# Performance work log

Hardware: AMD Instinct MI355X
Metric: run time of the kernel (lower is better)

The kernel has to match this reference:

```python
import jax, jax.numpy as jnp
import numpy as np

N = 20000      # nodes
E = 320000     # edges (avg degree 16)
IN = 64        # input feature dim
EMB = 128      # emb_dim / c_dim
OUT = 10       # num classes
L = 5          # num_layers
RATIO = 0.25
TEMP = 1.0
NOISE = 1.0
MAX_ITER = 30
EPS = 1e-20


def setup_inputs() -> dict:
    key = jax.random.key(0)
    ks = jax.random.split(key, 12)
    def w(k, shape, fan):
        return jax.random.normal(k, shape, jnp.float32) / np.float32(np.sqrt(fan))
    x = jax.random.normal(ks[0], (N, IN), jnp.float32)
    edge_index = jax.random.randint(ks[1], (2, E), 0, N, jnp.int32)
    u = jax.random.uniform(ks[2], (E, 1), jnp.float32)
    return {
        "x": x,
        "edge_index": edge_index,
        "u": u,
        "enc_W0": w(ks[3], (IN, EMB), IN), "enc_b0": jnp.zeros((EMB,), jnp.float32),
        "enc_W": w(ks[4], (L - 1, EMB, EMB), EMB), "enc_b": jnp.zeros((L - 1, EMB), jnp.float32),
        "ea_W1": w(ks[5], (2 * EMB, 4 * EMB), 2 * EMB), "ea_b1": jnp.zeros((4 * EMB,), jnp.float32),
        "ea_W2": w(ks[6], (4 * EMB, 1), 4 * EMB), "ea_b2": jnp.zeros((1,), jnp.float32),
        "cls_W0": w(ks[7], (IN, EMB), IN), "cls_b0": jnp.zeros((EMB,), jnp.float32),
        "cls_W": w(ks[8], (L - 1, EMB, EMB), EMB), "cls_b": jnp.zeros((L - 1, EMB), jnp.float32),
        "head_W": w(ks[9], (EMB, OUT), EMB), "head_b": jnp.zeros((OUT,), jnp.float32),
    }


def _gin_stack(x, W0, b0, Ws, bs, src, dst, att):
    """GIN-style stack: aggregate att-weighted neighbor messages, then linear+ReLU."""
    agg = jax.ops.segment_sum(x[src] * att, dst, num_segments=N)
    h = jax.nn.relu((x + agg) @ W0 + b0)
    def layer(h, wb):
        W, b = wb
        agg = jax.ops.segment_sum(h[src] * att, dst, num_segments=N)
        return jax.nn.relu((h + agg) @ W + b), None
    h, _ = jax.lax.scan(layer, h, (Ws, bs))
    return h


def reference(x, edge_index, u, enc_W0, enc_b0, enc_W, enc_b,
              ea_W1, ea_b1, ea_W2, ea_b2,
              cls_W0, cls_b0, cls_W, cls_b, head_W, head_b):
    src, dst = edge_index[0], edge_index[1]
    ones = jnp.ones((E, 1), jnp.float32)

    # GNN encoder
    h = _gin_stack(x, enc_W0, enc_b0, enc_W, enc_b, src, dst, ones)

    # edge attention MLP on [h_src, h_dst]
    edge_rep = jnp.concatenate([h[src], h[dst]], axis=-1)            # [E, 2*EMB]
    pe = jax.nn.relu(edge_rep @ ea_W1 + ea_b1) @ ea_W2 + ea_b2       # [E, 1]
    atts = (pe - pe.mean()) / jnp.std(pe, ddof=1)

    # Gumbel noise from uniform u (training path)
    g = -jnp.log(-jnp.log(u + EPS) + EPS)
    d = atts + g * NOISE

    s_min, s_max = atts.min(), atts.max()
    D = jnp.concatenate([d - s_min, s_max - d], axis=-1)             # [E, 2]
    logT = -D / TEMP
    log_rs = jnp.log(jnp.array([[E * (1.0 - RATIO), E * RATIO]], jnp.float32) + EPS)

    # 30-step Sinkhorn normalization in log space
    def body(i, lt):
        lt = lt - jax.scipy.special.logsumexp(lt, axis=-1, keepdims=True)
        lt = lt - jax.scipy.special.logsumexp(lt, axis=-2, keepdims=True)
        return lt + log_rs
    logT = jax.lax.fori_loop(0, MAX_ITER, body, logT)
    T = jnp.exp(logT)[:, 1:2]                                        # [E, 1]

    # classifier GNN on raw features with Sinkhorn edge attention
    hc = _gin_stack(x, cls_W0, cls_b0, cls_W, cls_b, src, dst, T)
    rep = hc.mean(axis=0)                                            # mean graph pooling
    return rep @ head_W + head_b                                     # [OUT]
```

## Files before the change

### kernel.cpp

```cpp
#include <hip/hip_runtime.h>
#include <math.h>

#define NN 20000
#define EE 320000
#define NBINS 2048
#define HRANGE 64.0f
#define EPSF 1e-20f

typedef __attribute__((ext_vector_type(8))) short bf16x8;
typedef __attribute__((ext_vector_type(4))) float f32x4;

constexpr size_t OFF_DEG  = 0;
constexpr size_t OFF_RS   = 20000;
constexpr size_t OFF_CUR  = 40008;
constexpr size_t OFF_EIX  = 60008;
constexpr size_t OFF_GSRC = 380008;
constexpr size_t OFF_B0   = 700008;
constexpr size_t OFF_B1   = 1980008;
constexpr size_t OFF_PA   = 3260008;
constexpr size_t OFF_PB   = 8380008;
constexpr size_t OFF_PE   = 13500008;
constexpr size_t OFF_DL   = 13820008;
constexpr size_t OFF_TT   = 14140008;
constexpr size_t OFF_HIST = 14460008;
constexpr size_t OFF_SCAL = 14464104;
constexpr size_t OFF_REP  = 14464136;
constexpr size_t OFF_WT   = 14464264;
constexpr size_t WT_ENC0 = 0;
constexpr size_t WT_ENC  = 8192;
constexpr size_t WT_CLS0 = 73728;
constexpr size_t WT_CLS  = 81920;
constexpr size_t WT_EA1  = 147456;

__device__ __forceinline__ unsigned ordf(float f) {
  unsigned b = __float_as_uint(f);
  return (b >> 31) ? ~b : (b | 0x80000000u);
}
__device__ __forceinline__ float unordf(unsigned u) {
  unsigned b = (u >> 31) ? (u ^ 0x80000000u) : ~u;
  return __uint_as_float(b);
}
__device__ __forceinline__ ushort f2bf(float f) {
  unsigned u = __float_as_uint(f);
  u += 0x7FFFu + ((u >> 16) & 1u);
  return (ushort)(u >> 16);
}
__device__ __forceinline__ unsigned pack2(float x, float y) {
  return (unsigned)f2bf(x) | ((unsigned)f2bf(y) << 16);
}
__device__ __forceinline__ float bf2f(ushort h) {
  return __uint_as_float(((unsigned)h) << 16);
}
__device__ __forceinline__ float bflo(unsigned v) { return __uint_as_float(v << 16); }
__device__ __forceinline__ float bfhi(unsigned v) { return __uint_as_float(v & 0xFFFF0000u); }

__global__ void init_ws(int* deg, int* cur, float* hist, float* scal, float* rep) {
  int i = blockIdx.x * blockDim.x + threadIdx.x;
  if (i < NN) { deg[i] = 0; cur[i] = 0; }
  if (i < 2 * NBINS) hist[i] = 0.f;
  if (i < 128) rep[i] = 0.f;
  if (i < 32) {
    if (i == 2)      ((unsigned*)scal)[2] = 0xFFFFFFFFu;
    else if (i == 3) ((unsigned*)scal)[3] = 0u;
    else scal[i] = 0.f;
  }
}

__global__ void count_deg(const int* __restrict__ dst, int* __restrict__ deg) {
  int e = blockIdx.x * 256 + threadIdx.x;
  if (e < EE) atomicAdd(&deg[dst[e]], 1);
}

__global__ __launch_bounds__(1024) void scan_deg(const int* __restrict__ deg,
                                                 int* __restrict__ rs) {
  __shared__ int ps[1024];
  const int t = threadIdx.x;
  const int base = t * 20;
  int loc[20];
  int s = 0;
#pragma unroll
  for (int j = 0; j < 20; ++j) {
    int idx = base + j;
    int v = (idx < NN) ? deg[idx] : 0;
    loc[j] = s;
    s += v;
  }
  ps[t] = s;
  __syncthreads();
  for (int off = 1; off < 1024; off <<= 1) {
    int x = (t >= off) ? ps[t - off] : 0;
    __syncthreads();
    ps[t] += x;
    __syncthreads();
  }
  const int excl = ps[t] - s;
#pragma unroll
  for (int j = 0; j < 20; ++j) {
    int idx = base + j;
    if (idx < NN) rs[idx] = excl + loc[j];
  }
  if (t == 1023) rs[NN] = ps[1023];
}

__global__ void fill_csr(const int* __restrict__ src, const int* __restrict__ dst,
                         const int* __restrict__ rs, int* __restrict__ cur,
                         int* __restrict__ eidx, int* __restrict__ gsrc) {
  int e = blockIdx.x * 256 + threadIdx.x;
  if (e < EE) {
    int d = dst[e];
    int p = atomicAdd(&cur[d], 1);
    int o = rs[d] + p;
    eidx[o] = e;
    gsrc[o] = src[e];
  }
}

__global__ void transpose_all(const float* __restrict__ encW0, const float* __restrict__ encW,
                              const float* __restrict__ clsW0, const float* __restrict__ clsW,
                              const float* __restrict__ eaW1, ushort* __restrict__ Wt) {
  int i = blockIdx.x * 256 + threadIdx.x;
  if (i < 8192) {
    int k = i >> 7, n = i & 127;
    Wt[WT_ENC0 + n * 64 + k] = f2bf(encW0[i]);
  } else if (i < 73728) {
    int j = i - 8192;
    int l = j >> 14, r = j & 16383, k = r >> 7, n = r & 127;
    Wt[WT_ENC + l * 16384 + n * 128 + k] = f2bf(encW[j]);
  } else if (i < 81920) {
    int j = i - 73728;
    int k = j >> 7, n = j & 127;
    Wt[WT_CLS0 + n * 64 + k] = f2bf(clsW0[j]);
  } else if (i < 147456) {
    int j = i - 81920;
    int l = j >> 14, r = j & 16383, k = r >> 7, n = r & 127;
    Wt[WT_CLS + l * 16384 + n * 128 + k] = f2bf(clsW[j]);
  } else if (i < 278528) {
    int j = i - 147456;
    int k = j >> 9, n = j & 511;
    Wt[WT_EA1 + n * 256 + k] = f2bf(eaW1[j]);
  }
}

template <bool HASATT>
__global__ __launch_bounds__(256) void fused_layer64(
    const float* __restrict__ X, ushort* __restrict__ C,
    const int* __restrict__ gsrc, const int* __restrict__ rs,
    const float* __restrict__ att, const ushort* __restrict__ Bt,
    const float* __restrict__ bias) {
  __shared__ __align__(16) char smem[8448];
  ushort* Asm = (ushort*)smem;
  const int tid = threadIdx.x;
  const int g = tid >> 4, l = tid & 15;
  const int nb = blockIdx.x * 16;
  {
    const int n = nb + g;
    const int e0 = rs[n];
    const int deg = rs[n + 1] - e0;
    float4 s = ((const float4*)(X + (size_t)n * 64))[l];
    float a[4] = {s.x, s.y, s.z, s.w};
    const float4* Xr = (const float4*)X;

    int i0 = gsrc[min(e0 + 0, EE - 1)];
    int i1 = gsrc[min(e0 + 1, EE - 1)];
    int i2 = gsrc[min(e0 + 2, EE - 1)];
    int i3 = gsrc[min(e0 + 3, EE - 1)];
    float4 F0 = Xr[(size_t)i0 * 16 + l];
    float4 F1 = Xr[(size_t)i1 * 16 + l];
    float4 F2 = Xr[(size_t)i2 * 16 + l];
    float4 F3 = Xr[(size_t)i3 * 16 + l];
    int G0 = gsrc[min(e0 + 4, EE - 1)];
    int G1 = gsrc[min(e0 + 5, EE - 1)];
    int G2 = gsrc[min(e0 + 6, EE - 1)];
    int G3 = gsrc[min(e0 + 7, EE - 1)];
    float W0 = 1.f, W1 = 1.f, W2 = 1.f, W3 = 1.f;
    if (HASATT) {
      W0 = att[min(e0 + 0, EE - 1)];
      W1 = att[min(e0 + 1, EE - 1)];
      W2 = att[min(e0 + 2, EE - 1)];
      W3 = att[min(e0 + 3, EE - 1)];
    }

#define FL64_STEP(F, G, W, J)                                                 \
    {                                                                         \
      if ((J) < deg) {                                                        \
        const float cw_ = HASATT ? (W) : 1.f;                                 \
        a[0] = fmaf(cw_, F.x, a[0]); a[1] = fmaf(cw_, F.y, a[1]);             \
        a[2] = fmaf(cw_, F.z, a[2]); a[3] = fmaf(cw_, F.w, a[3]);             \
      }                                                                       \
      F = Xr[(size_t)G * 16 + l];                                             \
      G = gsrc[min(e0 + (J) + 8, EE - 1)];                                    \
      if (HASATT) W = att[min(e0 + (J) + 4, EE - 1)];                         \
    }

    for (int j = 0; j < deg; j += 4) {
      FL64_STEP(F0, G0, W0, j);
      FL64_STEP(F1, G1, W1, j + 1);
      FL64_STEP(F2, G2, W2, j + 2);
      FL64_STEP(F3, G3, W3, j + 3);
    }
#undef FL64_STEP
    ushort4 o;
    o.x = f2bf(a[0]); o.y = f2bf(a[1]); o.z = f2bf(a[2]); o.w = f2bf(a[3]);
    *(ushort4*)(Asm + g * 72 + l * 4) = o;
  }
  __syncthreads();
  const int wave = tid >> 6, lane = tid & 63, quad = lane >> 4, l15 = lane & 15;
  f32x4 acc[2] = {{0.f, 0.f, 0.f, 0.f}, {0.f, 0.f, 0.f, 0.f}};
#pragma unroll
  for (int k0 = 0; k0 < 64; k0 += 32) {
    bf16x8 af = *(const bf16x8*)(Asm + l15 * 72 + k0 + quad * 8);
#pragma unroll
    for (int t = 0; t < 2; ++t) {
      int bn = wave * 32 + t * 16 + l15;
      bf16x8 bf = *(const bf16x8*)(Bt + (size_t)bn * 64 + k0 + quad * 8);
      acc[t] = __builtin_amdgcn_mfma_f32_16x16x32_bf16(af, bf, acc[t], 0, 0, 0);
    }
  }
  __syncthreads();
  float (*Csm)[132] = (float(*)[132])smem;
#pragma unroll
  for (int t = 0; t < 2; ++t) {
    int lc = wave * 32 + t * 16 + l15;
    float bs = bias[lc];
#pragma unroll
    for (int r = 0; r < 4; ++r)
      Csm[quad * 4 + r][lc] = fmaxf(acc[t][r] + bs, 0.f);
  }
  __syncthreads();
  const int r = tid >> 4, cc = (tid & 15) * 8;
  f32x4 v0 = *(const f32x4*)&Csm[r][cc];
  f32x4 v1 = *(const f32x4*)&Csm[r][cc + 4];
  uint4 o;
  o.x = pack2(v0[0], v0[1]); o.y = pack2(v0[2], v0[3]);
  o.z = pack2(v1[0], v1[1]); o.w = pack2(v1[2], v1[3]);
  *(uint4*)(C + (size_t)(nb + r) * 128 + cc) = o;
}

template <bool HASATT>
__global__ __launch_bounds__(256) void fused_layer128(
    const ushort* __restrict__ Xb, ushort* __restrict__ C,
    const int* __restrict__ gsrc, const int* __restrict__ rs,
    const float* __restrict__ att, const ushort* __restrict__ Bt,
    const float* __restrict__ bias) {
  __shared__ __align__(16) char smem[8448];
  ushort* Asm = (ushort*)smem;
  const int tid = threadIdx.x;
  const int g = tid >> 4, l = tid & 15;
  const int nb = blockIdx.x * 16;
  {
    const int n = nb + g;
    const int e0 = rs[n];
    const int deg = rs[n + 1] - e0;
    float a[8];
    {
      uint4 s = ((const uint4*)(Xb + (size_t)n * 128))[l];
      a[0] = bflo(s.x); a[1] = bfhi(s.x); a[2] = bflo(s.y); a[3] = bfhi(s.y);
      a[4] = bflo(s.z); a[5] = bfhi(s.z); a[6] = bflo(s.w); a[7] = bfhi(s.w);
    }
    const uint4* Xr = (const uint4*)Xb;

    int i0 = gsrc[min(e0 + 0, EE - 1)];
    int i1 = gsrc[min(e0 + 1, EE - 1)];
    int i2 = gsrc[min(e0 + 2, EE - 1)];
    int i3 = gsrc[min(e0 + 3, EE - 1)];
    uint4 F0 = Xr[(size_t)i0 * 16 + l];
    uint4 F1 = Xr[(size_t)i1 * 16 + l];
    uint4 F2 = Xr[(size_t)i2 * 16 + l];
    uint4 F3 = Xr[(size_t)i3 * 16 + l];
    int G0 = gsrc[min(e0 + 4, EE - 1)];
    int G1 = gsrc[min(e0 + 5, EE - 1)];
    int G2 = gsrc[min(e0 + 6, EE - 1)];
    int G3 = gsrc[min(e0 + 7, EE - 1)];
    float W0 = 1.f, W1 = 1.f, W2 = 1.f, W3 = 1.f;
    if (HASATT) {
      W0 = att[min(e0 + 0, EE - 1)];
      W1 = att[min(e0 + 1, EE - 1)];
      W2 = att[min(e0 + 2, EE - 1)];
      W3 = att[min(e0 + 3, EE - 1)];
    }

#define FL128_STEP(F, G, W, J)                                                \
    {                                                                         \
      if ((J) < deg) {                                                        \
        const float cw_ = HASATT ? (W) : 1.f;                                 \
        a[0] = fmaf(cw_, bflo(F.x), a[0]); a[1] = fmaf(cw_, bfhi(F.x), a[1]); \
        a[2] = fmaf(cw_, bflo(F.y), a[2]); a[3] = fmaf(cw_, bfhi(F.y), a[3]); \
        a[4] = fmaf(cw_, bflo(F.z), a[4]); a[5] = fmaf(cw_, bfhi(F.z), a[5]); \
        a[6] = fmaf(cw_, bflo(F.w), a[6]); a[7] = fmaf(cw_, bfhi(F.w), a[7]); \
      }                                                                       \
      F = Xr[(size_t)G * 16 + l];                                             \
      G = gsrc[min(e0 + (J) + 8, EE - 1)];                                    \
      if (HASATT) W = att[min(e0 + (J) + 4, EE - 1)];                         \
    }

    for (int j = 0; j < deg; j += 4) {
      FL128_STEP(F0, G0, W0, j);
      FL128_STEP(F1, G1, W1, j + 1);
      FL128_STEP(F2, G2, W2, j + 2);
      FL128_STEP(F3, G3, W3, j + 3);
    }
#undef FL128_STEP
    uint4 o;
    o.x = pack2(a[0], a[1]); o.y = pack2(a[2], a[3]);
    o.z = pack2(a[4], a[5]); o.w = pack2(a[6], a[7]);
    *(uint4*)(Asm + g * 136 + l * 8) = o;
  }
  __syncthreads();
  const int wave = tid >> 6, lane = tid & 63, quad = lane >> 4, l15 = lane & 15;
  f32x4 acc[2] = {{0.f, 0.f, 0.f, 0.f}, {0.f, 0.f, 0.f, 0.f}};
#pragma unroll
  for (int k0 = 0; k0 < 128; k0 += 32) {
    bf16x8 af = *(const bf16x8*)(Asm + l15 * 136 + k0 + quad * 8);
#pragma unroll
    for (int t = 0; t < 2; ++t) {
      int bn = wave * 32 + t * 16 + l15;
      bf16x8 bf = *(const bf16x8*)(Bt + (size_t)bn * 128 + k0 + quad * 8);
      acc[t] = __builtin_amdgcn_mfma_f32_16x16x32_bf16(af, bf, acc[t], 0, 0, 0);
    }
  }
  __syncthreads();
  float (*Csm)[132] = (float(*)[132])smem;
#pragma unroll
  for (int t = 0; t < 2; ++t) {
    int lc = wave * 32 + t * 16 + l15;
    float bs = bias[lc];
#pragma unroll
    for (int r = 0; r < 4; ++r)
      Csm[quad * 4 + r][lc] = fmaxf(acc[t][r] + bs, 0.f);
  }
  __syncthreads();
  const int r = tid >> 4, cc = (tid & 15) * 8;
  f32x4 v0 = *(const f32x4*)&Csm[r][cc];
  f32x4 v1 = *(const f32x4*)&Csm[r][cc + 4];
  uint4 o;
  o.x = pack2(v0[0], v0[1]); o.y = pack2(v0[2], v0[3]);
  o.z = pack2(v1[0], v1[1]); o.w = pack2(v1[2], v1[3]);
  *(uint4*)(C + (size_t)(nb + r) * 128 + cc) = o;
}

__global__ __launch_bounds__(256) void gemm_papb(
    const ushort* __restrict__ Hb, const ushort* __restrict__ W1t,
    const float* __restrict__ b1, ushort* __restrict__ Pa, ushort* __restrict__ Pb) {
  __shared__ float lds[32][132];
  const int tid = threadIdx.x;
  const int wave = tid >> 6, lane = tid & 63, quad = lane >> 4, l15 = lane & 15;
  const int mh = wave >> 1, nh = wave & 1;
  const bool isB = blockIdx.x >= 4;
  const int col0 = (blockIdx.x & 3) * 128;
  const int row0 = blockIdx.y * 32;
  const ushort* Bt = W1t + (isB ? 128 : 0);
  ushort* C = isB ? Pb : Pa;
  f32x4 acc[4] = {{0.f, 0.f, 0.f, 0.f}, {0.f, 0.f, 0.f, 0.f},
                  {0.f, 0.f, 0.f, 0.f}, {0.f, 0.f, 0.f, 0.f}};
  const ushort* Ap = Hb + (size_t)(row0 + mh * 16 + l15) * 128 + quad * 8;
#pragma unroll
  for (int k0 = 0; k0 < 128; k0 += 32) {
    bf16x8 af = *(const bf16x8*)(Ap + k0);
#pragma unroll
    for (int t = 0; t < 4; ++t) {
      int bn = col0 + nh * 64 + t * 16 + l15;
      bf16x8 bf = *(const bf16x8*)(Bt + (size_t)bn * 256 + k0 + quad * 8);
      acc[t] = __builtin_amdgcn_mfma_f32_16x16x32_bf16(af, bf, acc[t], 0, 0, 0);
    }
  }
#pragma unroll
  for (int t = 0; t < 4; ++t) {
    int lc = nh * 64 + t * 16 + l15;
    float bs = isB ? 0.f : b1[col0 + lc];
#pragma unroll
    for (int r = 0; r < 4; ++r)
      lds[mh * 16 + quad * 4 + r][lc] = acc[t][r] + bs;
  }
  __syncthreads();
  const int r = tid >> 3, c0 = (tid & 7) * 16;
  ushort* Cp = C + (size_t)(row0 + r) * 512 + col0 + c0;
#pragma unroll
  for (int k = 0; k < 4; ++k) {
    f32x4 v = *(const f32x4*)&lds[r][c0 + k * 4];
    ushort4 o;
    o.x = f2bf(v[0]); o.y = f2bf(v[1]); o.z = f2bf(v[2]); o.w = f2bf(v[3]);
    *(ushort4*)(Cp + k * 4) = o;
  }
}

__global__ __launch_bounds__(256) void edge_pe_csr(
    const ushort* __restrict__ Pa, const ushort* __restrict__ Pb,
    const int* __restrict__ gsrc, const int* __restrict__ rs,
    const float* __restrict__ W2, const float* __restrict__ b2,
    float* __restrict__ pe) {
  const int lane = threadIdx.x & 63;
  const int n = blockIdx.x * 4 + (threadIdx.x >> 6);
  const int e0 = rs[n];
  const int deg = rs[n + 1] - e0;
  if (deg <= 0) return;
  float w[8], pb[8];
  {
    const float4* w2v = (const float4*)(W2 + lane * 8);
    float4 t0 = w2v[0], t1 = w2v[1];
    w[0] = t0.x; w[1] = t0.y; w[2] = t0.z; w[3] = t0.w;
    w[4] = t1.x; w[5] = t1.y; w[6] = t1.z; w[7] = t1.w;
    uint4 b = ((const uint4*)(Pb + (size_t)n * 512))[lane];
    pb[0] = bflo(b.x); pb[1] = bfhi(b.x); pb[2] = bflo(b.y); pb[3] = bfhi(b.y);
    pb[4] = bflo(b.z); pb[5] = bfhi(b.z); pb[6] = bflo(b.w); pb[7] = bfhi(b.w);
  }
  const float b2v = b2[0];
  const uint4* Par = (const uint4*)Pa;

  int i0 = gsrc[min(e0 + 0, EE - 1)];
  int i1 = gsrc[min(e0 + 1, EE - 1)];
  int i2 = gsrc[min(e0 + 2, EE - 1)];
  int i3 = gsrc[min(e0 + 3, EE - 1)];
  uint4 F0 = Par[(size_t)i0 * 64 + lane];
  uint4 F1 = Par[(size_t)i1 * 64 + lane];
  uint4 F2 = Par[(size_t)i2 * 64 + lane];
  uint4 F3 = Par[(size_t)i3 * 64 + lane];
  int G0 = gsrc[min(e0 + 4, EE - 1)];
  int G1 = gsrc[min(e0 + 5, EE - 1)];
  int G2 = gsrc[min(e0 + 6, EE - 1)];
  int G3 = gsrc[min(e0 + 7, EE - 1)];

#define PE_STEP(F, G, J)                                                      \
  {                                                                           \
    if ((J) < deg) {                                                          \
      float pa[8] = {bflo(F.x), bfhi(F.x), bflo(F.y), bfhi(F.y),              \
                     bflo(F.z), bfhi(F.z), bflo(F.w), bfhi(F.w)};             \
      float acc = 0.f;                                                        \
      _Pragma("unroll")                                                       \
      for (int jj = 0; jj < 8; ++jj) acc += fmaxf(pa[jj] + pb[jj], 0.f) * w[jj]; \
      _Pragma("unroll")                                                       \
      for (int off = 32; off; off >>= 1) acc += __shfl_xor(acc, off);         \
      if (lane == 0) pe[e0 + (J)] = acc + b2v;                                \
    }                                                                         \
    F = Par[(size_t)G * 64 + lane];                                           \
    G = gsrc[min(e0 + (J) + 8, EE - 1)];                                      \
  }

  for (int j = 0; j < deg; j += 4) {
    PE_STEP(F0, G0, j);
    PE_STEP(F1, G1, j + 1);
    PE_STEP(F2, G2, j + 2);
    PE_STEP(F3, G3, j + 3);
  }
#undef PE_STEP
}

__global__ __launch_bounds__(256) void pe_stats(const float* __restrict__ pe,
                                                float* __restrict__ scal) {
  __shared__ float r1[256], r2[256], r3[256], r4[256];
  int tid = threadIdx.x;
  float s = 0.f, q = 0.f, mn = 3.0e38f, mx = -3.0e38f;
  for (int i = blockIdx.x * 256 + tid; i < EE; i += gridDim.x * 256) {
    float v = pe[i];
    s += v; q = fmaf(v, v, q);
    mn = fminf(mn, v); mx = fmaxf(mx, v);
  }
  r1[tid] = s; r2[tid] = q; r3[tid] = mn; r4[tid] = mx;
  __syncthreads();
  for (int k = 128; k > 0; k >>= 1) {
    if (tid < k) {
      r1[tid] += r1[tid + k];
      r2[tid] += r2[tid + k];
      r3[tid] = fminf(r3[tid], r3[tid + k]);
      r4[tid] = fmaxf(r4[tid], r4[tid + k]);
    }
    __syncthreads();
  }
  if (tid == 0) {
    unsafeAtomicAdd(&scal[0], r1[0]);
    unsafeAtomicAdd(&scal[1], r2[0]);
    atomicMin((unsigned*)scal + 2, ordf(r3[0]));
    atomicMax((unsigned*)scal + 3, ordf(r4[0]));
  }
}

__global__ __launch_bounds__(256) void edge_delta_hist(
    const float* __restrict__ pe, const float* __restrict__ u,
    const int* __restrict__ eidx, float* __restrict__ delta,
    float* __restrict__ hist, const float* __restrict__ scal) {
  __shared__ float cnt_s[NBINS], sum_s[NBINS];
  for (int b = threadIdx.x; b < NBINS; b += 256) { cnt_s[b] = 0.f; sum_s[b] = 0.f; }
  float sum = scal[0], ssq = scal[1];
  float mn = unordf(((const unsigned*)scal)[2]);
  float mx = unordf(((const unsigned*)scal)[3]);
  float mu = sum / (float)EE;
  float var = (ssq - sum * sum / (float)EE) / (float)(EE - 1);
  float istd = rsqrtf(fmaxf(var, 1e-30f));
  float shift = (mn - mu) * istd + (mx - mu) * istd;
  __syncthreads();
  for (int i = blockIdx.x * 256 + threadIdx.x; i < EE; i += gridDim.x * 256) {
    float uu = u[eidx[i]];
    float atts = (pe[i] - mu) * istd;
    float g = -logf(-logf(uu + EPSF) + EPSF);
    float dl = 2.0f * (atts + g) - shift;
    delta[i] = dl;
    float dcl = fminf(fmaxf(dl, -HRANGE), HRANGE * 0.9999f);
    int b = (int)((dcl + HRANGE) * ((float)NBINS / (2.0f * HRANGE)));
    b = min(max(b, 0), NBINS - 1);
    atomicAdd(&cnt_s[b], 1.0f);
    atomicAdd(&sum_s[b], dcl);
  }
  __syncthreads();
  for (int b = threadIdx.x; b < NBINS; b += 256) {
    float c = cnt_s[b];
    if (c != 0.f) {
      unsafeAtomicAdd(&hist[b], c);
      unsafeAtomicAdd(&hist[NBINS + b], sum_s[b]);
    }
  }
}

__global__ __launch_bounds__(64) void sinkhorn_iter(const float* __restrict__ hist,
                                                    float* __restrict__ scal) {
  const int lane = threadIdx.x;
  float cnt[32], mean[32];
#pragma unroll
  for (int b = 0; b < 32; ++b) {
    int idx = b * 64 + lane;
    float c = hist[idx];
    cnt[b] = c;
    mean[b] = (c > 0.f) ? hist[NBINS + idx] / c : 0.f;
  }
  const float LRD = -1.0986122886681098f;
  float S = 0.f, Zfin = 0.f;
  for (int it = 0; it < 30; ++it) {
    float p = 0.f;
#pragma unroll
    for (int b = 0; b < 32; ++b)
      if (cnt[b] > 0.f) p += cnt[b] / (1.f + expf(-(mean[b] + S)));
#pragma unroll
    for (int off = 32; off; off >>= 1) p += __shfl_xor(p, off);
    if (it < 29)
      S += logf(fmaxf((float)EE - p, 1.0f)) - logf(p) + LRD;
    else
      Zfin = p;
  }
  if (lane == 0) {
    scal[8] = S;
    scal[9] = ((float)EE * 0.25f) / Zfin;
  }
}

__global__ void compute_T(const float* __restrict__ delta,
                          const float* __restrict__ scal,
                          float* __restrict__ Ta) {
  int i = blockIdx.x * 256 + threadIdx.x;
  if (i >= EE) return;
  float S = scal[8], sc = scal[9];
  Ta[i] = sc / (1.f + expf(-(delta[i] + S)));
}

__global__ __launch_bounds__(128) void col_mean(const ushort* __restrict__ Hc,
                                                float* __restrict__ rep) {
  int c = threadIdx.x;
  const int g = gridDim.x;
  float p0 = 0.f, p1 = 0.f, p2 = 0.f, p3 = 0.f;
  int n = blockIdx.x;
  for (; n + 3 * g < NN; n += 4 * g) {
    p0 += bf2f(Hc[(size_t)n * 128 + c]);
    p1 += bf2f(Hc[(size_t)(n + g) * 128 + c]);
    p2 += bf2f(Hc[(size_t)(n + 2 * g) * 128 + c]);
    p3 += bf2f(Hc[(size_t)(n + 3 * g) * 128 + c]);
  }
  for (; n < NN; n += g) p0 += bf2f(Hc[(size_t)n * 128 + c]);
  unsafeAtomicAdd(&rep[c], (p0 + p1) + (p2 + p3));
}

__global__ __launch_bounds__(128) void head_kernel(const float* __restrict__ repsum,
                                                   const float* __restrict__ hW,
                                                   const float* __restrict__ hb,
                                                   float* __restrict__ out) {
  __shared__ float rep[128];
  int tid = threadIdx.x;
  if (tid < 128) rep[tid] = repsum[tid] * (1.0f / (float)NN);
  __syncthreads();
  if (tid < 10) {
    float a = hb[tid];
#pragma unroll
    for (int c = 0; c < 128; c++) a = fmaf(rep[c], hW[c * 10 + tid], a);
    out[tid] = a;
  }
}

extern "C" void kernel_launch(void* const* d_in, const int* in_sizes, int n_in,
                              void* d_out, int out_size, void* d_ws, size_t ws_size,
                              hipStream_t stream) {
  const float* x      = (const float*)d_in[0];
  const int*   ei     = (const int*)d_in[1];
  const float* u      = (const float*)d_in[2];
  const float* enc_W0 = (const float*)d_in[3];
  const float* enc_b0 = (const float*)d_in[4];
  const float* enc_W  = (const float*)d_in[5];
  const float* enc_b  = (const float*)d_in[6];
  const float* ea_W1  = (const float*)d_in[7];
  const float* ea_b1  = (const float*)d_in[8];
  const float* ea_W2  = (const float*)d_in[9];
  const float* ea_b2  = (const float*)d_in[10];
  const float* cls_W0 = (const float*)d_in[11];
  const float* cls_b0 = (const float*)d_in[12];
  const float* cls_W  = (const float*)d_in[13];
  const float* cls_b  = (const float*)d_in[14];
  const float* head_W = (const float*)d_in[15];
  const float* head_b = (const float*)d_in[16];
  const int* src  = ei;
  const int* dstp = ei + EE;

  float* wsF = (float*)d_ws;
  int*   wsI = (int*)d_ws;
  int* deg  = wsI + OFF_DEG;
  int* rs   = wsI + OFF_RS;
  int* cur  = wsI + OFF_CUR;
  int* eix  = wsI + OFF_EIX;
  int* gsrc = wsI + OFF_GSRC;
  ushort* B0 = (ushort*)(wsF + OFF_B0);
  ushort* B1 = (ushort*)(wsF + OFF_B1);
  ushort* Pa = (ushort*)(wsF + OFF_PA);
  ushort* Pb = (ushort*)(wsF + OFF_PB);
  float* pe   = wsF + OFF_PE;
  float* dl   = wsF + OFF_DL;
  float* Ta   = wsF + OFF_TT;
  float* hist = wsF + OFF_HIST;
  float* scal = wsF + OFF_SCAL;
  float* rep  = wsF + OFF_REP;
  ushort* Wt  = (ushort*)(wsF + OFF_WT);
  float* out = (float*)d_out;

  init_ws<<<(NN + 255) / 256, 256, 0, stream>>>(deg, cur, hist, scal, rep);
  count_deg<<<(EE + 255) / 256, 256, 0, stream>>>(dstp, deg);
  scan_deg<<<1, 1024, 0, stream>>>(deg, rs);
  fill_csr<<<(EE + 255) / 256, 256, 0, stream>>>(src, dstp, rs, cur, eix, gsrc);
  transpose_all<<<1088, 256, 0, stream>>>(enc_W0, enc_W, cls_W0, cls_W, ea_W1, Wt);

  const int GB = NN / 16;

  fused_layer64<false><<<GB, 256, 0, stream>>>(x, B0, gsrc, rs, nullptr, Wt + WT_ENC0, enc_b0);
  {
    ushort* in = B0; ushort* outb = B1;
    for (int l = 0; l < 4; l++) {
      fused_layer128<false><<<GB, 256, 0, stream>>>(in, outb, gsrc, rs, nullptr,
                                                    Wt + WT_ENC + (size_t)l * 16384,
                                                    enc_b + (size_t)l * 128);
      ushort* t = in; in = outb; outb = t;
    }
  }

  gemm_papb<<<dim3(8, NN / 32), 256, 0, stream>>>(B0, Wt + WT_EA1, ea_b1, Pa, Pb);
  edge_pe_csr<<<NN / 4, 256, 0, stream>>>(Pa, Pb, gsrc, rs, ea_W2, ea_b2, pe);

  pe_stats<<<512, 256, 0, stream>>>(pe, scal);
  edge_delta_hist<<<128, 256, 0, stream>>>(pe, u, eix, dl, hist, scal);
  sinkhorn_iter<<<1, 64, 0, stream>>>(hist, scal);
  compute_T<<<(EE + 255) / 256, 256, 0, stream>>>(dl, scal, Ta);

  fused_layer64<true><<<GB, 256, 0, stream>>>(x, B0, gsrc, rs, Ta, Wt + WT_CLS0, cls_b0);
  {
    ushort* in = B0; ushort* outb = B1;
    for (int l = 0; l < 4; l++) {
      fused_layer128<true><<<GB, 256, 0, stream>>>(in, outb, gsrc, rs, Ta,
                                                   Wt + WT_CLS + (size_t)l * 16384,
                                                   cls_b + (size_t)l * 128);
      ushort* t = in; in = outb; outb = t;
    }
  }

  col_mean<<<256, 128, 0, stream>>>(B0, rep);
  head_kernel<<<1, 128, 0, stream>>>(rep, head_W, head_b, out);
}
```

Measured before the change: 535.8 us.

## Compute edge attention scores with one thread per edge instead of one wave per node

Replaces the wave-per-destination-node edge scoring kernel, which used cross-lane shuffles and per-node gathers, with a thread-per-edge kernel. Each thread walks the full 512-wide Pa and Pb rows itself and accumulates the ReLU dot product. To support this, the CSR fill now also writes a per-edge destination array, stored in the T buffer region, which is only written later. This removes the shuffle reductions and the load imbalance from uneven degrees. In exchange, each thread makes strided, uncoalesced 16-byte loads across rows and no longer reuses Pb across edges held in registers, so memory efficiency depends on cache hits.

```diff
diff --git a/kernel.cpp b/kernel.cpp
--- a/kernel.cpp
+++ b/kernel.cpp
@@ -104,7 +104,8 @@
 
 __global__ void fill_csr(const int* __restrict__ src, const int* __restrict__ dst,
                          const int* __restrict__ rs, int* __restrict__ cur,
-                         int* __restrict__ eidx, int* __restrict__ gsrc) {
+                         int* __restrict__ eidx, int* __restrict__ gsrc,
+                         int* __restrict__ gdst) {
   int e = blockIdx.x * 256 + threadIdx.x;
   if (e < EE) {
     int d = dst[e];
@@ -112,6 +113,7 @@
     int o = rs[d] + p;
     eidx[o] = e;
     gsrc[o] = src[e];
+    gdst[o] = d;
   }
 }
 
@@ -385,63 +387,31 @@
 
 __global__ __launch_bounds__(256) void edge_pe_csr(
     const ushort* __restrict__ Pa, const ushort* __restrict__ Pb,
-    const int* __restrict__ gsrc, const int* __restrict__ rs,
+    const int* __restrict__ gsrc, const int* __restrict__ gdst,
     const float* __restrict__ W2, const float* __restrict__ b2,
     float* __restrict__ pe) {
-  const int lane = threadIdx.x & 63;
-  const int n = blockIdx.x * 4 + (threadIdx.x >> 6);
-  const int e0 = rs[n];
-  const int deg = rs[n + 1] - e0;
-  if (deg <= 0) return;
-  float w[8], pb[8];
-  {
-    const float4* w2v = (const float4*)(W2 + lane * 8);
-    float4 t0 = w2v[0], t1 = w2v[1];
-    w[0] = t0.x; w[1] = t0.y; w[2] = t0.z; w[3] = t0.w;
-    w[4] = t1.x; w[5] = t1.y; w[6] = t1.z; w[7] = t1.w;
-    uint4 b = ((const uint4*)(Pb + (size_t)n * 512))[lane];
-    pb[0] = bflo(b.x); pb[1] = bfhi(b.x); pb[2] = bflo(b.y); pb[3] = bfhi(b.y);
-    pb[4] = bflo(b.z); pb[5] = bfhi(b.z); pb[6] = bflo(b.w); pb[7] = bfhi(b.w);
-  }
-  const float b2v = b2[0];
-  const uint4* Par = (const uint4*)Pa;
-
-  int i0 = gsrc[min(e0 + 0, EE - 1)];
-  int i1 = gsrc[min(e0 + 1, EE - 1)];
-  int i2 = gsrc[min(e0 + 2, EE - 1)];
-  int i3 = gsrc[min(e0 + 3, EE - 1)];
-  uint4 F0 = Par[(size_t)i0 * 64 + lane];
-  uint4 F1 = Par[(size_t)i1 * 64 + lane];
-  uint4 F2 = Par[(size_t)i2 * 64 + lane];
-  uint4 F3 = Par[(size_t)i3 * 64 + lane];
-  int G0 = gsrc[min(e0 + 4, EE - 1)];
-  int G1 = gsrc[min(e0 + 5, EE - 1)];
-  int G2 = gsrc[min(e0 + 6, EE - 1)];
-  int G3 = gsrc[min(e0 + 7, EE - 1)];
-
-#define PE_STEP(F, G, J)                                                      \
-  {                                                                           \
-    if ((J) < deg) {                                                          \
-      float pa[8] = {bflo(F.x), bfhi(F.x), bflo(F.y), bfhi(F.y),              \
-                     bflo(F.z), bfhi(F.z), bflo(F.w), bfhi(F.w)};             \
-      float acc = 0.f;                                                        \
-      _Pragma("unroll")                                                       \
-      for (int jj = 0; jj < 8; ++jj) acc += fmaxf(pa[jj] + pb[jj], 0.f) * w[jj]; \
-      _Pragma("unroll")                                                       \
-      for (int off = 32; off; off >>= 1) acc += __shfl_xor(acc, off);         \
-      if (lane == 0) pe[e0 + (J)] = acc + b2v;                                \
-    }                                                                         \
-    F = Par[(size_t)G * 64 + lane];                                           \
-    G = gsrc[min(e0 + (J) + 8, EE - 1)];                                      \
-  }
-
-  for (int j = 0; j < deg; j += 4) {
-    PE_STEP(F0, G0, j);
-    PE_STEP(F1, G1, j + 1);
-    PE_STEP(F2, G2, j + 2);
-    PE_STEP(F3, G3, j + 3);
-  }
-#undef PE_STEP
+  const int e = blockIdx.x * 256 + threadIdx.x;
+  const int s = gsrc[e], d = gdst[e];
+  const uint4* Par = (const uint4*)(Pa + (size_t)s * 512);
+  const uint4* Pbr = (const uint4*)(Pb + (size_t)d * 512);
+  const float4* Wv = (const float4*)W2;
+  float a0 = 0.f, a1 = 0.f, a2 = 0.f, a3 = 0.f;
+#pragma unroll 8
+  for (int c = 0; c < 64; ++c) {
+    uint4 pa = Par[c];
+    uint4 pb = Pbr[c];
+    float4 w0 = Wv[c * 2], w1 = Wv[c * 2 + 1];
+    float t;
+    t = fmaxf(bflo(pa.x) + bflo(pb.x), 0.f); a0 = fmaf(t, w0.x, a0);
+    t = fmaxf(bfhi(pa.x) + bfhi(pb.x), 0.f); a1 = fmaf(t, w0.y, a1);
+    t = fmaxf(bflo(pa.y) + bflo(pb.y), 0.f); a2 = fmaf(t, w0.z, a2);
+    t = fmaxf(bfhi(pa.y) + bfhi(pb.y), 0.f); a3 = fmaf(t, w0.w, a3);
+    t = fmaxf(bflo(pa.z) + bflo(pb.z), 0.f); a0 = fmaf(t, w1.x, a0);
+    t = fmaxf(bfhi(pa.z) + bfhi(pb.z), 0.f); a1 = fmaf(t, w1.y, a1);
+    t = fmaxf(bflo(pa.w) + bflo(pb.w), 0.f); a2 = fmaf(t, w1.z, a2);
+    t = fmaxf(bfhi(pa.w) + bfhi(pb.w), 0.f); a3 = fmaf(t, w1.w, a3);
+  }
+  pe[e] = ((a0 + a1) + (a2 + a3)) + b2[0];
 }
 
 __global__ __launch_bounds__(256) void pe_stats(const float* __restrict__ pe,
@@ -611,6 +581,7 @@
   int* cur  = wsI + OFF_CUR;
   int* eix  = wsI + OFF_EIX;
   int* gsrc = wsI + OFF_GSRC;
+  int* gdst = wsI + OFF_TT;
   ushort* B0 = (ushort*)(wsF + OFF_B0);
   ushort* B1 = (ushort*)(wsF + OFF_B1);
   ushort* Pa = (ushort*)(wsF + OFF_PA);
@@ -627,7 +598,7 @@
   init_ws<<<(NN + 255) / 256, 256, 0, stream>>>(deg, cur, hist, scal, rep);
   count_deg<<<(EE + 255) / 256, 256, 0, stream>>>(dstp, deg);
   scan_deg<<<1, 1024, 0, stream>>>(deg, rs);
-  fill_csr<<<(EE + 255) / 256, 256, 0, stream>>>(src, dstp, rs, cur, eix, gsrc);
+  fill_csr<<<(EE + 255) / 256, 256, 0, stream>>>(src, dstp, rs, cur, eix, gsrc, gdst);
   transpose_all<<<1088, 256, 0, stream>>>(enc_W0, enc_W, cls_W0, cls_W, ea_W1, Wt);
 
   const int GB = NN / 16;
@@ -644,7 +615,7 @@
   }
 
   gemm_papb<<<dim3(8, NN / 32), 256, 0, stream>>>(B0, Wt + WT_EA1, ea_b1, Pa, Pb);
-  edge_pe_csr<<<NN / 4, 256, 0, stream>>>(Pa, Pb, gsrc, rs, ea_W2, ea_b2, pe);
+  edge_pe_csr<<<EE / 256, 256, 0, stream>>>(Pa, Pb, gsrc, gdst, ea_W2, ea_b2, pe);
 
   pe_stats<<<512, 256, 0, stream>>>(pe, scal);
   edge_delta_hist<<<128, 256, 0, stream>>>(pe, u, eix, dl, hist, scal);
```

Result: slower. 547.3 us (+2.1%).

## Assign one wavefront per node in GIN layers with quad-split edge gathering

Applied to the files above, without the earlier changes.

The fused aggregate-plus-GEMM layer kernels now process 4 nodes per block instead of 16. Each wavefront owns one node, and its four 16-lane quads walk interleaved edge subsets, then combine their partial sums with cross-lane shuffles. This targets load imbalance from varying node degrees, which previously made whole waves wait on the slowest of four nodes. The cost is that the 16-row MFMA tile now carries only 4 useful rows, there are four times as many blocks reloading the weight tile, and each lane has less gather prefetch depth.

```diff
diff --git a/kernel.cpp b/kernel.cpp
--- a/kernel.cpp
+++ b/kernel.cpp
@@ -150,61 +150,54 @@
   __shared__ __align__(16) char smem[8448];
   ushort* Asm = (ushort*)smem;
   const int tid = threadIdx.x;
-  const int g = tid >> 4, l = tid & 15;
-  const int nb = blockIdx.x * 16;
+  const int wave = tid >> 6, lane = tid & 63;
+  const int c = lane & 15;
+  const int q = lane >> 4;
+  const int nb = blockIdx.x * 4;
   {
-    const int n = nb + g;
-    const int e0 = rs[n];
-    const int deg = rs[n + 1] - e0;
-    float4 s = ((const float4*)(X + (size_t)n * 64))[l];
-    float a[4] = {s.x, s.y, s.z, s.w};
+    const int n = nb + wave;
+    const int e0 = rs[n], e1 = rs[n + 1];
+    const int deg = e1 - e0;
     const float4* Xr = (const float4*)X;
-
-    int i0 = gsrc[min(e0 + 0, EE - 1)];
-    int i1 = gsrc[min(e0 + 1, EE - 1)];
-    int i2 = gsrc[min(e0 + 2, EE - 1)];
-    int i3 = gsrc[min(e0 + 3, EE - 1)];
-    float4 F0 = Xr[(size_t)i0 * 16 + l];
-    float4 F1 = Xr[(size_t)i1 * 16 + l];
-    float4 F2 = Xr[(size_t)i2 * 16 + l];
-    float4 F3 = Xr[(size_t)i3 * 16 + l];
-    int G0 = gsrc[min(e0 + 4, EE - 1)];
-    int G1 = gsrc[min(e0 + 5, EE - 1)];
-    int G2 = gsrc[min(e0 + 6, EE - 1)];
-    int G3 = gsrc[min(e0 + 7, EE - 1)];
-    float W0 = 1.f, W1 = 1.f, W2 = 1.f, W3 = 1.f;
+    float a[4];
+    {
+      float4 s = Xr[(size_t)n * 16 + c];
+      if (q == 0) { a[0] = s.x; a[1] = s.y; a[2] = s.z; a[3] = s.w; }
+      else        { a[0] = 0.f; a[1] = 0.f; a[2] = 0.f; a[3] = 0.f; }
+    }
+    const int base = e0 + q;
+    int i0 = gsrc[min(base, EE - 1)];
+    float4 F = Xr[(size_t)i0 * 16 + c];
+    int G = gsrc[min(base + 4, EE - 1)];
+    float W = 1.f, Wn = 1.f;
     if (HASATT) {
-      W0 = att[min(e0 + 0, EE - 1)];
-      W1 = att[min(e0 + 1, EE - 1)];
-      W2 = att[min(e0 + 2, EE - 1)];
-      W3 = att[min(e0 + 3, EE - 1)];
-    }
-
-#define FL64_STEP(F, G, W, J)                                                 \
-    {                                                                         \
-      if ((J) < deg) {                                                        \
-        const float cw_ = HASATT ? (W) : 1.f;                                 \
-        a[0] = fmaf(cw_, F.x, a[0]); a[1] = fmaf(cw_, F.y, a[1]);             \
-        a[2] = fmaf(cw_, F.z, a[2]); a[3] = fmaf(cw_, F.w, a[3]);             \
-      }                                                                       \
-      F = Xr[(size_t)G * 16 + l];                                             \
-      G = gsrc[min(e0 + (J) + 8, EE - 1)];                                    \
-      if (HASATT) W = att[min(e0 + (J) + 4, EE - 1)];                         \
-    }
-
-    for (int j = 0; j < deg; j += 4) {
-      FL64_STEP(F0, G0, W0, j);
-      FL64_STEP(F1, G1, W1, j + 1);
-      FL64_STEP(F2, G2, W2, j + 2);
-      FL64_STEP(F3, G3, W3, j + 3);
-    }
-#undef FL64_STEP
-    ushort4 o;
-    o.x = f2bf(a[0]); o.y = f2bf(a[1]); o.z = f2bf(a[2]); o.w = f2bf(a[3]);
-    *(ushort4*)(Asm + g * 72 + l * 4) = o;
-  }
-  __syncthreads();
-  const int wave = tid >> 6, lane = tid & 63, quad = lane >> 4, l15 = lane & 15;
+      W  = att[min(base, EE - 1)];
+      Wn = att[min(base + 4, EE - 1)];
+    }
+    const int nit = (deg + 3) >> 2;
+    for (int it = 0; it < nit; ++it) {
+      if (base + it * 4 < e1) {
+        const float w_ = HASATT ? W : 1.f;
+        a[0] = fmaf(w_, F.x, a[0]); a[1] = fmaf(w_, F.y, a[1]);
+        a[2] = fmaf(w_, F.z, a[2]); a[3] = fmaf(w_, F.w, a[3]);
+      }
+      F = Xr[(size_t)G * 16 + c];
+      G = gsrc[min(base + (it + 2) * 4, EE - 1)];
+      if (HASATT) { W = Wn; Wn = att[min(base + (it + 2) * 4, EE - 1)]; }
+    }
+#pragma unroll
+    for (int j = 0; j < 4; ++j) {
+      a[j] += __shfl_xor(a[j], 16);
+      a[j] += __shfl_xor(a[j], 32);
+    }
+    if (q == 0) {
+      ushort4 o;
+      o.x = f2bf(a[0]); o.y = f2bf(a[1]); o.z = f2bf(a[2]); o.w = f2bf(a[3]);
+      *(ushort4*)(Asm + wave * 72 + c * 4) = o;
+    }
+  }
+  __syncthreads();
+  const int quad = lane >> 4, l15 = lane & 15;
   f32x4 acc[2] = {{0.f, 0.f, 0.f, 0.f}, {0.f, 0.f, 0.f, 0.f}};
 #pragma unroll
   for (int k0 = 0; k0 < 64; k0 += 32) {
@@ -228,12 +221,14 @@
   }
   __syncthreads();
   const int r = tid >> 4, cc = (tid & 15) * 8;
-  f32x4 v0 = *(const f32x4*)&Csm[r][cc];
-  f32x4 v1 = *(const f32x4*)&Csm[r][cc + 4];
-  uint4 o;
-  o.x = pack2(v0[0], v0[1]); o.y = pack2(v0[2], v0[3]);
-  o.z = pack2(v1[0], v1[1]); o.w = pack2(v1[2], v1[3]);
-  *(uint4*)(C + (size_t)(nb + r) * 128 + cc) = o;
+  if (r < 4) {
+    f32x4 v0 = *(const f32x4*)&Csm[r][cc];
+    f32x4 v1 = *(const f32x4*)&Csm[r][cc + 4];
+    uint4 o;
+    o.x = pack2(v0[0], v0[1]); o.y = pack2(v0[2], v0[3]);
+    o.z = pack2(v1[0], v1[1]); o.w = pack2(v1[2], v1[3]);
+    *(uint4*)(C + (size_t)(nb + r) * 128 + cc) = o;
+  }
 }
 
 template <bool HASATT>
@@ -245,68 +240,62 @@
   __shared__ __align__(16) char smem[8448];
   ushort* Asm = (ushort*)smem;
   const int tid = threadIdx.x;
-  const int g = tid >> 4, l = tid & 15;
-  const int nb = blockIdx.x * 16;
+  const int wave = tid >> 6, lane = tid & 63;
+  const int c = lane & 15;
+  const int q = lane >> 4;
+  const int nb = blockIdx.x * 4;
   {
-    const int n = nb + g;
-    const int e0 = rs[n];
-    const int deg = rs[n + 1] - e0;
+    const int n = nb + wave;
+    const int e0 = rs[n], e1 = rs[n + 1];
+    const int deg = e1 - e0;
+    const uint4* Xr = (const uint4*)Xb;
     float a[8];
     {
-      uint4 s = ((const uint4*)(Xb + (size_t)n * 128))[l];
-      a[0] = bflo(s.x); a[1] = bfhi(s.x); a[2] = bflo(s.y); a[3] = bfhi(s.y);
-      a[4] = bflo(s.z); a[5] = bfhi(s.z); a[6] = bflo(s.w); a[7] = bfhi(s.w);
-    }
-    const uint4* Xr = (const uint4*)Xb;
-
-    int i0 = gsrc[min(e0 + 0, EE - 1)];
-    int i1 = gsrc[min(e0 + 1, EE - 1)];
-    int i2 = gsrc[min(e0 + 2, EE - 1)];
-    int i3 = gsrc[min(e0 + 3, EE - 1)];
-    uint4 F0 = Xr[(size_t)i0 * 16 + l];
-    uint4 F1 = Xr[(size_t)i1 * 16 + l];
-    uint4 F2 = Xr[(size_t)i2 * 16 + l];
-    uint4 F3 = Xr[(size_t)i3 * 16 + l];
-    int G0 = gsrc[min(e0 + 4, EE - 1)];
-    int G1 = gsrc[min(e0 + 5, EE - 1)];
-    int G2 = gsrc[min(e0 + 6, EE - 1)];
-    int G3 = gsrc[min(e0 + 7, EE - 1)];
-    float W0 = 1.f, W1 = 1.f, W2 = 1.f, W3 = 1.f;
+      uint4 s = Xr[(size_t)n * 16 + c];
+      if (q == 0) {
+        a[0] = bflo(s.x); a[1] = bfhi(s.x); a[2] = bflo(s.y); a[3] = bfhi(s.y);
+        a[4] = bflo(s.z); a[5] = bfhi(s.z); a[6] = bflo(s.w); a[7] = bfhi(s.w);
+      } else {
+#pragma unroll
+        for (int j = 0; j < 8; ++j) a[j] = 0.f;
+      }
+    }
+    const int base = e0 + q;
+    int i0 = gsrc[min(base, EE - 1)];
+    uint4 F = Xr[(size_t)i0 * 16 + c];
+    int G = gsrc[min(base + 4, EE - 1)];
+    float W = 1.f, Wn = 1.f;
     if (HASATT) {
-      W0 = att[min(e0 + 0, EE - 1)];
-      W1 = att[min(e0 + 1, EE - 1)];
-      W2 = att[min(e0 + 2, EE - 1)];
-      W3 = att[min(e0 + 3, EE - 1)];
-    }
-
-#define FL128_STEP(F, G, W, J)                                                \
-    {                                                                         \
-      if ((J) < deg) {                                                        \
-        const float cw_ = HASATT ? (W) : 1.f;                                 \
-        a[0] = fmaf(cw_, bflo(F.x), a[0]); a[1] = fmaf(cw_, bfhi(F.x), a[1]); \
-        a[2] = fmaf(cw_, bflo(F.y), a[2]); a[3] = fmaf(cw_, bfhi(F.y), a[3]); \
-        a[4] = fmaf(cw_, bflo(F.z), a[4]); a[5] = fmaf(cw_, bfhi(F.z), a[5]); \
-        a[6] = fmaf(cw_, bflo(F.w), a[6]); a[7] = fmaf(cw_, bfhi(F.w), a[7]); \
-      }                                                                       \
-      F = Xr[(size_t)G * 16 + l];                                             \
-      G = gsrc[min(e0 + (J) + 8, EE - 1)];                                    \
-      if (HASATT) W = att[min(e0 + (J) + 4, EE - 1)];                         \
-    }
-
-    for (int j = 0; j < deg; j += 4) {
-      FL128_STEP(F0, G0, W0, j);
-      FL128_STEP(F1, G1, W1, j + 1);
-      FL128_STEP(F2, G2, W2, j + 2);
-      FL128_STEP(F3, G3, W3, j + 3);
-    }
-#undef FL128_STEP
-    uint4 o;
-    o.x = pack2(a[0], a[1]); o.y = pack2(a[2], a[3]);
-    o.z = pack2(a[4], a[5]); o.w = pack2(a[6], a[7]);
-    *(uint4*)(Asm + g * 136 + l * 8) = o;
-  }
-  __syncthreads();
-  const int wave = tid >> 6, lane = tid & 63, quad = lane >> 4, l15 = lane & 15;
+      W  = att[min(base, EE - 1)];
+      Wn = att[min(base + 4, EE - 1)];
+    }
+    const int nit = (deg + 3) >> 2;
+    for (int it = 0; it < nit; ++it) {
+      if (base + it * 4 < e1) {
+        const float w_ = HASATT ? W : 1.f;
+        a[0] = fmaf(w_, bflo(F.x), a[0]); a[1] = fmaf(w_, bfhi(F.x), a[1]);
+        a[2] = fmaf(w_, bflo(F.y), a[2]); a[3] = fmaf(w_, bfhi(F.y), a[3]);
+        a[4] = fmaf(w_, bflo(F.z), a[4]); a[5] = fmaf(w_, bfhi(F.z), a[5]);
+        a[6] = fmaf(w_, bflo(F.w), a[6]); a[7] = fmaf(w_, bfhi(F.w), a[7]);
+      }
+      F = Xr[(size_t)G * 16 + c];
+      G = gsrc[min(base + (it + 2) * 4, EE - 1)];
+      if (HASATT) { W = Wn; Wn = att[min(base + (it + 2) * 4, EE - 1)]; }
+    }
+#pragma unroll
+    for (int j = 0; j < 8; ++j) {
+      a[j] += __shfl_xor(a[j], 16);
+      a[j] += __shfl_xor(a[j], 32);
+    }
+    if (q == 0) {
+      uint4 o;
+      o.x = pack2(a[0], a[1]); o.y = pack2(a[2], a[3]);
+      o.z = pack2(a[4], a[5]); o.w = pack2(a[6], a[7]);
+      *(uint4*)(Asm + wave * 136 + c * 8) = o;
+    }
+  }
+  __syncthreads();
+  const int quad = lane >> 4, l15 = lane & 15;
   f32x4 acc[2] = {{0.f, 0.f, 0.f, 0.f}, {0.f, 0.f, 0.f, 0.f}};
 #pragma unroll
   for (int k0 = 0; k0 < 128; k0 += 32) {
@@ -330,12 +319,14 @@
   }
   __syncthreads();
   const int r = tid >> 4, cc = (tid & 15) * 8;
-  f32x4 v0 = *(const f32x4*)&Csm[r][cc];
-  f32x4 v1 = *(const f32x4*)&Csm[r][cc + 4];
-  uint4 o;
-  o.x = pack2(v0[0], v0[1]); o.y = pack2(v0[2], v0[3]);
-  o.z = pack2(v1[0], v1[1]); o.w = pack2(v1[2], v1[3]);
-  *(uint4*)(C + (size_t)(nb + r) * 128 + cc) = o;
+  if (r < 4) {
+    f32x4 v0 = *(const f32x4*)&Csm[r][cc];
+    f32x4 v1 = *(const f32x4*)&Csm[r][cc + 4];
+    uint4 o;
+    o.x = pack2(v0[0], v0[1]); o.y = pack2(v0[2], v0[3]);
+    o.z = pack2(v1[0], v1[1]); o.w = pack2(v1[2], v1[3]);
+    *(uint4*)(C + (size_t)(nb + r) * 128 + cc) = o;
+  }
 }
 
 __global__ __launch_bounds__(256) void gemm_papb(
@@ -630,7 +621,7 @@
   fill_csr<<<(EE + 255) / 256, 256, 0, stream>>>(src, dstp, rs, cur, eix, gsrc);
   transpose_all<<<1088, 256, 0, stream>>>(enc_W0, enc_W, cls_W0, cls_W, ea_W1, Wt);
 
-  const int GB = NN / 16;
+  const int GB = NN / 4;
 
   fused_layer64<false><<<GB, 256, 0, stream>>>(x, B0, gsrc, rs, nullptr, Wt + WT_ENC0, enc_b0);
   {
```

Result: slower. 665.4 us (+24.2%).
